# Performance work log

Measured on AMD Instinct MI355X. Metric: run time of the kernel, lower is better.

## Reference

```python
import jax, jax.numpy as jnp
import numpy as np

NUM_CLASSES = 80
S = 7            # grid_size
NB = 2           # num_boxes per cell
LAMBDA_COORD = 5.0
LAMBDA_NOOBJ = 0.5
N_BOX = 20       # padded boxes per image


def setup_inputs() -> dict:
    key = jax.random.key(0)
    k1, k2, k3, k4 = jax.random.split(key, 4)
    B = 4096
    predictions = jax.random.uniform(k1, (B, S, S, NB, 5 + NUM_CLASSES), dtype=jnp.float32)
    # build valid normalized xyxy boxes: centers in [0.1,0.9], half-sizes in [0.01,0.085]
    centers = jax.random.uniform(k2, (B, N_BOX, 2), dtype=jnp.float32) * 0.8 + 0.1
    half = jax.random.uniform(k3, (B, N_BOX, 2), dtype=jnp.float32) * 0.075 + 0.01
    targets_boxes = jnp.concatenate([centers - half, centers + half], axis=-1)
    targets_labels = jax.random.randint(k4, (B, N_BOX), 0, NUM_CLASSES)
    return {"predictions": predictions, "targets_boxes": targets_boxes, "targets_labels": targets_labels}


def encode_targets(boxes, labels):
    # boxes: [B,N,4] xyxy normalized; labels: [B,N] int
    B, N, _ = boxes.shape
    x = (boxes[..., 0] + boxes[..., 2]) * 0.5
    y = (boxes[..., 1] + boxes[..., 3]) * 0.5
    w = boxes[..., 2] - boxes[..., 0]
    h = boxes[..., 3] - boxes[..., 1]
    j = jnp.clip(jnp.floor(x * S).astype(jnp.int32), 0, S - 1)
    i = jnp.clip(jnp.floor(y * S).astype(jnp.int32), 0, S - 1)
    x_cell = x * S - j
    y_cell = y * S - i
    onehot = jax.nn.one_hot(labels, NUM_CLASSES, dtype=boxes.dtype)
    feats = jnp.concatenate([x_cell[..., None], y_cell[..., None], w[..., None], h[..., None],
                             jnp.ones_like(x_cell)[..., None], onehot], axis=-1)  # [B,N,5+C]
    bidx = jnp.arange(B, dtype=jnp.int32)[:, None]
    flat = ((bidx * S + i) * S + j).ravel()                       # [B*N] cell ids
    order = jnp.broadcast_to(jnp.arange(N, dtype=jnp.int32), (B, N)).ravel()
    winner = jnp.full((B * S * S,), N, dtype=jnp.int32).at[flat].min(order)
    cell_b = jnp.arange(B * S * S, dtype=jnp.int32) // (S * S)
    sel = jnp.minimum(winner, N - 1)
    grid = feats[cell_b, sel]
    grid = jnp.where((winner < N)[:, None], grid, jnp.zeros_like(grid))
    return grid.reshape(B, S, S, 5 + NUM_CLASSES)


def iou_xywh(a, b):
    ax1 = a[..., 0] - a[..., 2] * 0.5; ay1 = a[..., 1] - a[..., 3] * 0.5
    ax2 = a[..., 0] + a[..., 2] * 0.5; ay2 = a[..., 1] + a[..., 3] * 0.5
    bx1 = b[..., 0] - b[..., 2] * 0.5; by1 = b[..., 1] - b[..., 3] * 0.5
    bx2 = b[..., 0] + b[..., 2] * 0.5; by2 = b[..., 1] + b[..., 3] * 0.5
    iw = jnp.clip(jnp.minimum(ax2, bx2) - jnp.maximum(ax1, bx1), 0.0)
    ih = jnp.clip(jnp.minimum(ay2, by2) - jnp.maximum(ay1, by1), 0.0)
    inter = iw * ih
    union = (ax2 - ax1) * (ay2 - ay1) + (bx2 - bx1) * (by2 - by1) - inter
    return inter / (union + 1e-6)


def yolo_loss(predictions, targets_boxes, targets_labels):
    B = predictions.shape[0]
    tg = encode_targets(targets_boxes, targets_labels)   # [B,S,S,5+C]
    txy, twh = tg[..., :2], tg[..., 2:4]
    tconf, tcls = tg[..., 4:5], tg[..., 5:]
    obj = (tconf[..., 0] > 0).astype(predictions.dtype)   # [B,S,S]
    # responsible box = argmax IoU per cell, masked by obj
    pred_boxes = predictions[..., 0:4]                     # [B,S,S,NB,4]
    tgt_boxes = jnp.concatenate([txy, twh], axis=-1)[:, :, :, None, :]
    ious = iou_xywh(pred_boxes, jnp.broadcast_to(tgt_boxes, pred_boxes.shape))  # [B,S,S,NB]
    best = jnp.argmax(ious, axis=-1)
    resp = jax.nn.one_hot(best, NB, dtype=predictions.dtype) * obj[..., None]   # [B,S,S,NB]
    pxy = predictions[..., 0:2]; pwh = predictions[..., 2:4]
    pconf = predictions[..., 4:5]; pcls = predictions[..., 5:]
    om = obj[..., None, None]        # [B,S,S,1,1]
    rm = resp[..., None]             # [B,S,S,NB,1]
    loss_xy = LAMBDA_COORD * jnp.sum(om * rm * (pxy - txy[:, :, :, None, :]) ** 2) / B
    loss_wh = LAMBDA_COORD * jnp.sum(om * rm * (jnp.sqrt(jnp.clip(pwh, 1e-6)) - jnp.sqrt(jnp.clip(twh[:, :, :, None, :], 1e-6))) ** 2) / B
    loss_conf_obj = jnp.sum(om * rm * (pconf - tconf[:, :, :, None, :]) ** 2) / B
    loss_conf_noobj = LAMBDA_NOOBJ * jnp.sum((1.0 - obj)[..., None, None] * pconf ** 2) / B
    pred_cls_resp = jnp.sum(pcls * rm, axis=3)             # [B,S,S,C]
    loss_cls = jnp.sum(obj[..., None] * (pred_cls_resp - tcls) ** 2) / B
    return loss_xy + loss_wh + loss_conf_obj + loss_conf_noobj + loss_cls


def reference(predictions, targets_boxes, targets_labels):
    return yolo_loss(predictions, targets_boxes, targets_labels)
```

## Files before the change

kernel.cpp:

```cpp
#include <hip/hip_runtime.h>

#define S 7
#define NB 2
#define NC 80
#define NBOX 20
#define CELLS 49
#define CH 85
#define PAIR 170
#define PER_B 8330
#define N4 4165
#define L_COORD 5.0f
#define L_NOOBJ 0.5f

__device__ __forceinline__ float elem1(float p, unsigned c, int r,
                                       const float* __restrict__ wt)
{
    int nb  = (r >= CH) ? 1 : 0;
    int rr  = r - nb * CH;
    int cat = (rr >= 4) + (rr >= 5);
    float w = wt[c * 8u + (unsigned)(nb * 4 + cat)];
    return w * p * p;
}

__device__ __forceinline__ float elem4(float4 v, int e,
                                       const float* __restrict__ wt)
{
    unsigned ff = 4u * (unsigned)e;
    unsigned c0 = ff / (unsigned)PAIR;
    int r0 = (int)(ff - c0 * (unsigned)PAIR);
    int wrap = (r0 == PAIR - 2) ? 1 : 0;
    unsigned c1 = c0 + (unsigned)wrap;
    int r2 = wrap ? 0 : r0 + 2;
    float a;
    a  = elem1(v.x, c0, r0,     wt);
    a += elem1(v.y, c0, r0 + 1, wt);
    a += elem1(v.z, c1, r2,     wt);
    a += elem1(v.w, c1, r2 + 1, wt);
    return a;
}

__global__ __launch_bounds__(256) void yolo_loss_kernel(
    const float* __restrict__ pred,
    const float* __restrict__ boxes,
    const int*   __restrict__ labels,
    float*       __restrict__ out,
    float inv_B)
{
    __shared__ int   s_winner[2 * CELLS];
    __shared__ float s_cx[2 * NBOX], s_cy[2 * NBOX], s_bw[2 * NBOX], s_bh[2 * NBOX];
    __shared__ int   s_lab[2 * NBOX];
    __shared__ float s_wt[2 * CELLS * 8];
    __shared__ float s_wsum[4];

    const int b0  = blockIdx.x * 2;
    const int tid = threadIdx.x;

    if (tid < 2 * CELLS) s_winner[tid] = NBOX;
    __syncthreads();

    if (tid < 2 * NBOX) {
        int img = (tid >= NBOX) ? 1 : 0;
        const float* bx = boxes + ((size_t)(b0 + img) * NBOX + (tid - img * NBOX)) * 4;
        float x1 = bx[0], y1 = bx[1], x2 = bx[2], y2 = bx[3];
        float x = (x1 + x2) * 0.5f, y = (y1 + y2) * 0.5f;
        s_cx[tid] = x; s_cy[tid] = y;
        s_bw[tid] = x2 - x1; s_bh[tid] = y2 - y1;
        s_lab[tid] = labels[(size_t)(b0 + img) * NBOX + (tid - img * NBOX)];
        int j = (int)floorf(x * (float)S); j = min(max(j, 0), S - 1);
        int i = (int)floorf(y * (float)S); i = min(max(i, 0), S - 1);
        atomicMin(&s_winner[img * CELLS + i * S + j], tid - img * NBOX);
    }
    __syncthreads();

    float acc = 0.0f;
    if (tid < 2 * CELLS) {
        int img  = (tid >= CELLS) ? 1 : 0;
        int cell = tid - img * CELLS;
        int w    = s_winner[tid];
        int base = tid * 8;
        if (w < NBOX) {
            int i = cell / S, j = cell - (cell / S) * S;
            int bi = img * NBOX + w;
            float x = s_cx[bi], y = s_cy[bi];
            float tx = x * (float)S - (float)j;
            float ty = y * (float)S - (float)i;
            float tw = s_bw[bi], th = s_bh[bi];

            const float* p = pred + ((size_t)(b0 + img) * CELLS + cell) * PAIR;
            float bx1 = tx - tw * 0.5f, by1 = ty - th * 0.5f;
            float bx2 = tx + tw * 0.5f, by2 = ty + th * 0.5f;
            float barea = (bx2 - bx1) * (by2 - by1);
            float iou[2], px[2], py[2], pw[2], ph[2];
            #pragma unroll
            for (int nb = 0; nb < NB; nb++) {
                px[nb] = p[nb * CH + 0]; py[nb] = p[nb * CH + 1];
                pw[nb] = p[nb * CH + 2]; ph[nb] = p[nb * CH + 3];
                float ax1 = px[nb] - pw[nb] * 0.5f, ay1 = py[nb] - ph[nb] * 0.5f;
                float ax2 = px[nb] + pw[nb] * 0.5f, ay2 = py[nb] + ph[nb] * 0.5f;
                float iw = fmaxf(fminf(ax2, bx2) - fmaxf(ax1, bx1), 0.0f);
                float ih = fmaxf(fminf(ay2, by2) - fmaxf(ay1, by1), 0.0f);
                float inter = iw * ih;
                float uni = (ax2 - ax1) * (ay2 - ay1) + barea - inter;
                iou[nb] = inter / (uni + 1e-6f);
            }
            int resp = (iou[1] > iou[0]) ? 1 : 0;
            int oth  = 1 - resp;

            s_wt[base + resp * 4 + 0] = 0.0f;
            s_wt[base + resp * 4 + 1] = 1.0f;
            s_wt[base + resp * 4 + 2] = 1.0f;
            s_wt[base + oth  * 4 + 0] = 0.0f;
            s_wt[base + oth  * 4 + 1] = 0.0f;
            s_wt[base + oth  * 4 + 2] = 0.0f;

            float pc = p[resp * CH + 4];
            float pl = p[resp * CH + 5 + s_lab[bi]];
            float dx = px[resp] - tx, dy = py[resp] - ty;
            float dw = sqrtf(fmaxf(pw[resp], 1e-6f)) - sqrtf(fmaxf(tw, 1e-6f));
            float dh = sqrtf(fmaxf(ph[resp], 1e-6f)) - sqrtf(fmaxf(th, 1e-6f));
            acc = L_COORD * (dx * dx + dy * dy + dw * dw + dh * dh)
                + (1.0f - 2.0f * pc)
                + (1.0f - 2.0f * pl);
        } else {
            s_wt[base + 0] = 0.0f; s_wt[base + 1] = L_NOOBJ; s_wt[base + 2] = 0.0f;
            s_wt[base + 4] = 0.0f; s_wt[base + 5] = L_NOOBJ; s_wt[base + 6] = 0.0f;
        }
    }
    __syncthreads();

    const float4* p4 = (const float4*)(pred + (size_t)b0 * PER_B);
    #pragma unroll
    for (int k = 0; k < 16; ++k) {
        int e = tid + k * 256;
        float4 v = p4[e];
        acc += elem4(v, e, s_wt);
    }
    {
        int e = 4096 + tid;
        if (e < N4) acc += elem4(p4[e], e, s_wt);
    }

    #pragma unroll
    for (int off = 32; off > 0; off >>= 1) acc += __shfl_down(acc, off, 64);
    int lane = tid & 63, wv = tid >> 6;
    if (lane == 0) s_wsum[wv] = acc;
    __syncthreads();
    if (tid == 0) {
        float s = s_wsum[0] + s_wsum[1] + s_wsum[2] + s_wsum[3];
        atomicAdd(out, s * inv_B);
    }
}

extern "C" void kernel_launch(void* const* d_in, const int* in_sizes, int n_in,
                              void* d_out, int out_size, void* d_ws, size_t ws_size,
                              hipStream_t stream) {
    const float* pred   = (const float*)d_in[0];
    const float* boxes  = (const float*)d_in[1];
    const int*   labels = (const int*)d_in[2];

    const int B = in_sizes[0] / PER_B;

    hipMemsetAsync(d_out, 0, sizeof(float) * out_size, stream);
    yolo_loss_kernel<<<B / 2, 256, 0, stream>>>(pred, boxes, labels,
                                                (float*)d_out, 1.0f / (float)B);
}
```

Measured before the change: 213.9 us.

## Split loss into prep, grid-stride streaming, and final reduce kernels

Splits the fused per-pair-of-images kernel into three kernels. A prep kernel computes cell assignments and per-cell float4 weights into workspace. A streaming kernel reads predictions with a grid-wide stride and applies those weights. A single-block kernel reduces the partials, which removes the global atomicAdd and the memset. The aim is fully coalesced streaming without per-block setup stalls, at the cost of extra launches, a workspace round-trip for the weights, and a batch size hardcoded to 4096.

```diff
diff --git a/kernel.cpp b/kernel.cpp
--- a/kernel.cpp
+++ b/kernel.cpp
@@ -8,76 +8,66 @@
 #define CH 85
 #define PAIR 170
 #define PER_B 8330
-#define N4 4165
+#define NIMG 4096
+#define NCELL_TOT (NIMG*CELLS)
+#define N4TOT (NIMG*PER_B/4)
+#define PREP_IMGS 4
+#define PREP_BLOCKS (NIMG/PREP_IMGS)
+#define STREAM_BLOCKS 2048
+#define TSTRIDE (STREAM_BLOCKS*256)
 #define L_COORD 5.0f
 #define L_NOOBJ 0.5f
 
-__device__ __forceinline__ float elem1(float p, unsigned c, int r,
-                                       const float* __restrict__ wt)
+__device__ __forceinline__ void block_reduce_store(float acc, float* dst)
 {
-    int nb  = (r >= CH) ? 1 : 0;
-    int rr  = r - nb * CH;
-    int cat = (rr >= 4) + (rr >= 5);
-    float w = wt[c * 8u + (unsigned)(nb * 4 + cat)];
-    return w * p * p;
+    __shared__ float s_wsum[4];
+    int tid = threadIdx.x;
+    #pragma unroll
+    for (int off = 32; off > 0; off >>= 1) acc += __shfl_down(acc, off, 64);
+    int lane = tid & 63, wv = tid >> 6;
+    if (lane == 0) s_wsum[wv] = acc;
+    __syncthreads();
+    if (tid == 0) *dst = s_wsum[0] + s_wsum[1] + s_wsum[2] + s_wsum[3];
 }
 
-__device__ __forceinline__ float elem4(float4 v, int e,
-                                       const float* __restrict__ wt)
-{
-    unsigned ff = 4u * (unsigned)e;
-    unsigned c0 = ff / (unsigned)PAIR;
-    int r0 = (int)(ff - c0 * (unsigned)PAIR);
-    int wrap = (r0 == PAIR - 2) ? 1 : 0;
-    unsigned c1 = c0 + (unsigned)wrap;
-    int r2 = wrap ? 0 : r0 + 2;
-    float a;
-    a  = elem1(v.x, c0, r0,     wt);
-    a += elem1(v.y, c0, r0 + 1, wt);
-    a += elem1(v.z, c1, r2,     wt);
-    a += elem1(v.w, c1, r2 + 1, wt);
-    return a;
-}
-
-__global__ __launch_bounds__(256) void yolo_loss_kernel(
+__global__ __launch_bounds__(256) void prep_kernel(
     const float* __restrict__ pred,
     const float* __restrict__ boxes,
     const int*   __restrict__ labels,
-    float*       __restrict__ out,
-    float inv_B)
+    float4*      __restrict__ wt4,
+    float*       __restrict__ partial)
 {
-    __shared__ int   s_winner[2 * CELLS];
-    __shared__ float s_cx[2 * NBOX], s_cy[2 * NBOX], s_bw[2 * NBOX], s_bh[2 * NBOX];
-    __shared__ int   s_lab[2 * NBOX];
-    __shared__ float s_wt[2 * CELLS * 8];
-    __shared__ float s_wsum[4];
+    __shared__ int   s_winner[PREP_IMGS * CELLS];
+    __shared__ float s_cx[PREP_IMGS * NBOX], s_cy[PREP_IMGS * NBOX];
+    __shared__ float s_bw[PREP_IMGS * NBOX], s_bh[PREP_IMGS * NBOX];
+    __shared__ int   s_lab[PREP_IMGS * NBOX];
 
-    const int b0  = blockIdx.x * 2;
+    const int b0  = blockIdx.x * PREP_IMGS;
     const int tid = threadIdx.x;
 
-    if (tid < 2 * CELLS) s_winner[tid] = NBOX;
+    if (tid < PREP_IMGS * CELLS) s_winner[tid] = NBOX;
     __syncthreads();
 
-    if (tid < 2 * NBOX) {
-        int img = (tid >= NBOX) ? 1 : 0;
-        const float* bx = boxes + ((size_t)(b0 + img) * NBOX + (tid - img * NBOX)) * 4;
+    if (tid < PREP_IMGS * NBOX) {
+        int img = tid / NBOX, bxi = tid - img * NBOX;
+        const float* bx = boxes + ((size_t)(b0 + img) * NBOX + bxi) * 4;
         float x1 = bx[0], y1 = bx[1], x2 = bx[2], y2 = bx[3];
         float x = (x1 + x2) * 0.5f, y = (y1 + y2) * 0.5f;
         s_cx[tid] = x; s_cy[tid] = y;
         s_bw[tid] = x2 - x1; s_bh[tid] = y2 - y1;
-        s_lab[tid] = labels[(size_t)(b0 + img) * NBOX + (tid - img * NBOX)];
+        s_lab[tid] = labels[(size_t)(b0 + img) * NBOX + bxi];
         int j = (int)floorf(x * (float)S); j = min(max(j, 0), S - 1);
         int i = (int)floorf(y * (float)S); i = min(max(i, 0), S - 1);
-        atomicMin(&s_winner[img * CELLS + i * S + j], tid - img * NBOX);
+        atomicMin(&s_winner[img * CELLS + i * S + j], bxi);
     }
     __syncthreads();
 
     float acc = 0.0f;
-    if (tid < 2 * CELLS) {
-        int img  = (tid >= CELLS) ? 1 : 0;
+    if (tid < PREP_IMGS * CELLS) {
+        int img  = tid / CELLS;
         int cell = tid - img * CELLS;
         int w    = s_winner[tid];
-        int base = tid * 8;
+        float4 wq;
         if (w < NBOX) {
             int i = cell / S, j = cell - (cell / S) * S;
             int bi = img * NBOX + w;
@@ -104,14 +94,8 @@
                 iou[nb] = inter / (uni + 1e-6f);
             }
             int resp = (iou[1] > iou[0]) ? 1 : 0;
-            int oth  = 1 - resp;
-
-            s_wt[base + resp * 4 + 0] = 0.0f;
-            s_wt[base + resp * 4 + 1] = 1.0f;
-            s_wt[base + resp * 4 + 2] = 1.0f;
-            s_wt[base + oth  * 4 + 0] = 0.0f;
-            s_wt[base + oth  * 4 + 1] = 0.0f;
-            s_wt[base + oth  * 4 + 2] = 0.0f;
+            wq = (resp == 0) ? make_float4(1.f, 1.f, 0.f, 0.f)
+                             : make_float4(0.f, 0.f, 1.f, 1.f);
 
             float pc = p[resp * CH + 4];
             float pl = p[resp * CH + 5 + s_lab[bi]];
@@ -122,33 +106,77 @@
                 + (1.0f - 2.0f * pc)
                 + (1.0f - 2.0f * pl);
         } else {
-            s_wt[base + 0] = 0.0f; s_wt[base + 1] = L_NOOBJ; s_wt[base + 2] = 0.0f;
-            s_wt[base + 4] = 0.0f; s_wt[base + 5] = L_NOOBJ; s_wt[base + 6] = 0.0f;
+            wq = make_float4(L_NOOBJ, 0.f, L_NOOBJ, 0.f);
         }
+        wt4[(size_t)(b0 + img) * CELLS + cell] = wq;
     }
     __syncthreads();
+    block_reduce_store(acc, &partial[blockIdx.x]);
+}
 
-    const float4* p4 = (const float4*)(pred + (size_t)b0 * PER_B);
-    #pragma unroll
+__device__ __forceinline__ float elem1(float p, int r, float4 w)
+{
+    int nb = (r >= CH) ? 1 : 0;
+    int rr = r - nb * CH;
+    float wconf = nb ? w.z : w.x;
+    float wcls  = nb ? w.w : w.y;
+    float m = (rr >= 5) ? wcls : ((rr == 4) ? wconf : 0.0f);
+    return m * p * p;
+}
+
+__device__ __forceinline__ float elem4(float4 v, int e,
+                                       const float4* __restrict__ wt4)
+{
+    unsigned ff = 4u * (unsigned)e;
+    unsigned c0 = ff / (unsigned)PAIR;
+    int r0 = (int)(ff - c0 * (unsigned)PAIR);
+    float4 w0 = wt4[c0];
+    float4 w1 = w0;
+    bool wrap = (r0 == PAIR - 2);
+    if (wrap) w1 = wt4[c0 + 1];
+    int r2 = wrap ? 0 : r0 + 2;
+    float a;
+    a  = elem1(v.x, r0,     w0);
+    a += elem1(v.y, r0 + 1, w0);
+    a += elem1(v.z, r2,     w1);
+    a += elem1(v.w, r2 + 1, w1);
+    return a;
+}
+
+__global__ __launch_bounds__(256) void stream_kernel(
+    const float4* __restrict__ p4,
+    const float4* __restrict__ wt4,
+    float*        __restrict__ partial)
+{
+    const int tid = threadIdx.x;
+    const int gid = blockIdx.x * 256 + tid;
+
+    float acc = 0.0f;
+    int e = gid;
+    #pragma unroll 8
     for (int k = 0; k < 16; ++k) {
-        int e = tid + k * 256;
-        float4 v = p4[e];
-        acc += elem4(v, e, s_wt);
+        acc += elem4(p4[e], e, wt4);
+        e += TSTRIDE;
     }
-    {
-        int e = 4096 + tid;
-        if (e < N4) acc += elem4(p4[e], e, s_wt);
-    }
+    if (e < N4TOT) acc += elem4(p4[e], e, wt4);
 
+    block_reduce_store(acc, &partial[blockIdx.x]);
+}
+
+__global__ __launch_bounds__(256) void reduce_kernel(
+    const float* __restrict__ partial, int n,
+    float* __restrict__ out, float inv_B)
+{
+    const int tid = threadIdx.x;
+    float acc = 0.0f;
+    for (int i = tid; i < n; i += 256) acc += partial[i];
+    __shared__ float s_wsum[4];
     #pragma unroll
     for (int off = 32; off > 0; off >>= 1) acc += __shfl_down(acc, off, 64);
     int lane = tid & 63, wv = tid >> 6;
     if (lane == 0) s_wsum[wv] = acc;
     __syncthreads();
-    if (tid == 0) {
-        float s = s_wsum[0] + s_wsum[1] + s_wsum[2] + s_wsum[3];
-        atomicAdd(out, s * inv_B);
-    }
+    if (tid == 0) out[0] = (s_wsum[0] + s_wsum[1] + s_wsum[2] + s_wsum[3]) * inv_B;
 }
 
 extern "C" void kernel_launch(void* const* d_in, const int* in_sizes, int n_in,
@@ -158,9 +186,12 @@
     const float* boxes  = (const float*)d_in[1];
     const int*   labels = (const int*)d_in[2];
 
-    const int B = in_sizes[0] / PER_B;
+    float4* wt4          = (float4*)d_ws;
+    float*  prep_part    = (float*)d_ws + (size_t)NCELL_TOT * 4;
+    float*  stream_part  = prep_part + PREP_BLOCKS;
 
-    hipMemsetAsync(d_out, 0, sizeof(float) * out_size, stream);
-    yolo_loss_kernel<<<B / 2, 256, 0, stream>>>(pred, boxes, labels,
-                                                (float*)d_out, 1.0f / (float)B);
+    prep_kernel<<<PREP_BLOCKS, 256, 0, stream>>>(pred, boxes, labels, wt4, prep_part);
+    stream_kernel<<<STREAM_BLOCKS, 256, 0, stream>>>((const float4*)pred, wt4, stream_part);
+    reduce_kernel<<<1, 256, 0, stream>>>(prep_part, PREP_BLOCKS + STREAM_BLOCKS,
+                                         (float*)d_out, 1.0f / (float)NIMG);
 }
```

New measurement: 201.9 us. 1.06x faster.
